# Performance work log

Measured on AMD Instinct MI355X. Metric: run time of the kernel, lower is better.

The kernel has to match this reference:

```python
import jax, jax.numpy as jnp
import numpy as np

D = 1024  # 2 * hidden_size

def setup_inputs() -> dict:
    key = jax.random.key(0)
    ks = jax.random.split(key, 7)
    s = 1.0 / np.sqrt(D)
    return {
        "lstm_output": jax.random.normal(ks[0], (8, 2048, D), dtype=jnp.float32),
        "Wq": jax.random.uniform(ks[1], (D, D), jnp.float32, -s, s),
        "bq": jax.random.uniform(ks[2], (D,), jnp.float32, -s, s),
        "Wk": jax.random.uniform(ks[3], (D, D), jnp.float32, -s, s),
        "bk": jax.random.uniform(ks[4], (D,), jnp.float32, -s, s),
        "Wv": jax.random.uniform(ks[5], (D, D), jnp.float32, -s, s),
        "bv": jax.random.uniform(ks[6], (D,), jnp.float32, -s, s),
    }

def reference(lstm_output, Wq, bq, Wk, bk, Wv, bv):
    # x: [B, S, D]
    Q = lstm_output @ Wq + bq
    K = lstm_output @ Wk + bk
    V = lstm_output @ Wv + bv
    # Unscaled attention scores: [B, S, S]
    scores = jnp.einsum("bqd,bkd->bqk", Q, K)
    weights = jax.nn.softmax(scores, axis=-1)
    context = jnp.einsum("bqk,bkd->bqd", weights, V)
    return context
```

## Files before the change

### kernel.cpp

```cpp
#include <hip/hip_runtime.h>

typedef _Float16 half8 __attribute__((ext_vector_type(8)));
typedef _Float16 half4 __attribute__((ext_vector_type(4)));
typedef short short8 __attribute__((ext_vector_type(8)));
typedef unsigned short ushort4v __attribute__((ext_vector_type(4)));
typedef float floatx4 __attribute__((ext_vector_type(4)));

#define ASYNC16(g, l) __builtin_amdgcn_global_load_lds( \
    (const __attribute__((address_space(1))) void*)(g),  \
    (__attribute__((address_space(3))) void*)(l), 16, 0, 0)

__device__ inline unsigned short f2bf(float f) {
    unsigned u = __builtin_bit_cast(unsigned, f);
    u += 0x7fff + ((u >> 16) & 1);
    return (unsigned short)(u >> 16);
}
__device__ inline float bf2f(unsigned short b) {
    unsigned u = (unsigned)b << 16;
    return __builtin_bit_cast(float, u);
}

__global__ void cvt_f2h(const float* __restrict__ in, _Float16* __restrict__ out, int n4)
{
    int i = blockIdx.x * blockDim.x + threadIdx.x;
    const int stride = gridDim.x * blockDim.x;
    for (; i < n4; i += stride) {
        float4 v = ((const float4*)in)[i];
        half4 h = { (_Float16)v.x, (_Float16)v.y, (_Float16)v.z, (_Float16)v.w };
        ((half4*)out)[i] = h;
    }
}

__global__ void transpose_w(const float* __restrict__ Wq, const float* __restrict__ Wk,
                            const float* __restrict__ Wv, _Float16* __restrict__ Wt)
{
    const float* W = (blockIdx.z == 0) ? Wq : (blockIdx.z == 1) ? Wk : Wv;
    _Float16* out = Wt + (size_t)blockIdx.z * 1024 * 1024;
    __shared__ float t[32][33];
    const int tx = threadIdx.x, ty = threadIdx.y;
    const int k0 = blockIdx.x * 32, n0 = blockIdx.y * 32;
#pragma unroll
    for (int i = 0; i < 32; i += 8)
        t[ty + i][tx] = W[(size_t)(k0 + ty + i) * 1024 + n0 + tx];
    __syncthreads();
#pragma unroll
    for (int i = 0; i < 32; i += 8)
        out[(size_t)(n0 + ty + i) * 1024 + k0 + tx] = (_Float16)t[tx][ty + i];
}

__global__ __launch_bounds__(256, 2)
void gemm_qkv(const _Float16* __restrict__ X, const _Float16* __restrict__ Wt,
              const float* __restrict__ bq, const float* __restrict__ bk,
              const float* __restrict__ bv,
              _Float16* __restrict__ Qh, _Float16* __restrict__ Kh,
              unsigned short* __restrict__ Vt)
{
    __shared__ __align__(16) _Float16 sA[128 * 64];
    __shared__ __align__(16) _Float16 sB[128 * 64];
    const int tid = threadIdx.x;
    const int lane = tid & 63, wave = tid >> 6;
    const int quad = lane >> 4, l15 = lane & 15;
    const int wm = (wave & 1) * 64, wn = (wave >> 1) * 64;
    const long m0 = (long)blockIdx.y * 128;
    const int  n0 = blockIdx.x * 128;

    const _Float16* Ab = X + m0 * 1024;
    const _Float16* Bb = Wt + (long)n0 * 1024;

    long offA[4];
    int ldsOff[4];
#pragma unroll
    for (int u = 0; u < 4; ++u) {
        const int c = tid + u * 256;
        const int row = c >> 3, g = (c & 7) ^ (row & 7);
        offA[u] = (long)row * 1024 + g * 8;
        ldsOff[u] = c * 16;
    }
    const int sw = l15 & 7;

    floatx4 acc[4][4] = {};

    for (int k0 = 0; k0 < 1024; k0 += 64) {
        __syncthreads();
#pragma unroll
        for (int u = 0; u < 4; ++u) {
            ASYNC16(Ab + offA[u] + k0, (char*)sA + ldsOff[u]);
            ASYNC16(Bb + offA[u] + k0, (char*)sB + ldsOff[u]);
        }
        __syncthreads();
#pragma unroll
        for (int s = 0; s < 2; ++s) {
            const int ck = ((s * 4 + quad) ^ sw) * 8;
            half8 af[4], bf[4];
#pragma unroll
            for (int i = 0; i < 4; ++i) {
                af[i] = *(const half8*)(sA + (wm + i * 16 + l15) * 64 + ck);
                bf[i] = *(const half8*)(sB + (wn + i * 16 + l15) * 64 + ck);
            }
#pragma unroll
            for (int i = 0; i < 4; ++i)
#pragma unroll
                for (int j = 0; j < 4; ++j)
                    acc[i][j] = __builtin_amdgcn_mfma_f32_16x16x32_f16(af[i], bf[j], acc[i][j], 0, 0, 0);
        }
    }

    const int which = n0 >> 10;
    const int ncol0 = n0 & 1023;
    const float* bias = (which == 0) ? bq : (which == 1) ? bk : bv;

    if (which < 2) {
        _Float16* O = which ? Kh : Qh;
#pragma unroll
        for (int i = 0; i < 4; ++i) {
            const long mb = m0 + wm + i * 16 + quad * 4;
#pragma unroll
            for (int j = 0; j < 4; ++j) {
                const int col = ncol0 + wn + j * 16 + l15;
                const float bb = bias[col];
                _Float16* op = O + mb * 1024 + col;
#pragma unroll
                for (int r = 0; r < 4; ++r)
                    op[(long)r * 1024] = (_Float16)(acc[i][j][r] + bb);
            }
        }
    } else {
#pragma unroll
        for (int i = 0; i < 4; ++i) {
            const long mb = m0 + wm + i * 16 + quad * 4;
            const int b = (int)(mb >> 11);
            const int s = (int)(mb & 2047);
#pragma unroll
            for (int j = 0; j < 4; ++j) {
                const int col = ncol0 + wn + j * 16 + l15;
                const float bb = bias[col];
                ushort4v h;
#pragma unroll
                for (int r = 0; r < 4; ++r) h[r] = f2bf(acc[i][j][r] + bb);
                *(ushort4v*)(Vt + (long)b * 2097152 + (long)col * 2048 + s) = h;
            }
        }
    }
}

__global__ __launch_bounds__(256, 2)
void gemm_sc(const _Float16* __restrict__ Q, const _Float16* __restrict__ K,
             unsigned short* __restrict__ E, float* __restrict__ rowsum)
{
    __shared__ __align__(16) _Float16 sA[128 * 64];
    __shared__ __align__(16) _Float16 sB[128 * 64];
    const int tid = threadIdx.x;
    const int lane = tid & 63, wave = tid >> 6;
    const int quad = lane >> 4, l15 = lane & 15;
    const int wm = (wave & 1) * 64, wn = (wave >> 1) * 64;
    const long m0 = (long)blockIdx.y * 128;
    const long n0 = (long)blockIdx.x * 128;

    const _Float16* Ab = Q + (long)blockIdx.z * 2097152 + m0 * 1024;
    const _Float16* Bb = K + (long)blockIdx.z * 2097152 + n0 * 1024;
    unsigned short* Eb = E + (long)blockIdx.z * 4194304;
    float* rs = rowsum + (long)blockIdx.z * 2048;

    long offA[4];
    int ldsOff[4];
#pragma unroll
    for (int u = 0; u < 4; ++u) {
        const int c = tid + u * 256;
        const int row = c >> 3, g = (c & 7) ^ (row & 7);
        offA[u] = (long)row * 1024 + g * 8;
        ldsOff[u] = c * 16;
    }
    const int sw = l15 & 7;

    floatx4 acc[4][4] = {};

    for (int k0 = 0; k0 < 1024; k0 += 64) {
        __syncthreads();
#pragma unroll
        for (int u = 0; u < 4; ++u) {
            ASYNC16(Ab + offA[u] + k0, (char*)sA + ldsOff[u]);
            ASYNC16(Bb + offA[u] + k0, (char*)sB + ldsOff[u]);
        }
        __syncthreads();
#pragma unroll
        for (int s = 0; s < 2; ++s) {
            const int ck = ((s * 4 + quad) ^ sw) * 8;
            half8 af[4], bf[4];
#pragma unroll
            for (int i = 0; i < 4; ++i) {
                af[i] = *(const half8*)(sA + (wm + i * 16 + l15) * 64 + ck);
                bf[i] = *(const half8*)(sB + (wn + i * 16 + l15) * 64 + ck);
            }
#pragma unroll
            for (int i = 0; i < 4; ++i)
#pragma unroll
                for (int j = 0; j < 4; ++j)
                    acc[i][j] = __builtin_amdgcn_mfma_f32_16x16x32_f16(af[i], bf[j], acc[i][j], 0, 0, 0);
        }
    }

#pragma unroll
    for (int i = 0; i < 4; ++i) {
        const int rowb = (int)(m0 + wm + i * 16 + quad * 4);
#pragma unroll
        for (int r = 0; r < 4; ++r) {
            float sl = 0.f;
#pragma unroll
            for (int j = 0; j < 4; ++j) {
                const long col = n0 + wn + j * 16 + l15;
                unsigned short b = f2bf(__expf(acc[i][j][r] - 40.0f));
                Eb[(long)(rowb + r) * 2048 + col] = b;
                sl += bf2f(b);
            }
            sl += __shfl_xor(sl, 1);
            sl += __shfl_xor(sl, 2);
            sl += __shfl_xor(sl, 4);
            sl += __shfl_xor(sl, 8);
            if (l15 == 0) atomicAdd(&rs[rowb + r], sl);
        }
    }
}

__global__ __launch_bounds__(256, 2)
void gemm_pv(const unsigned short* __restrict__ E, const unsigned short* __restrict__ Vt,
             const float* __restrict__ rowsum, float* __restrict__ C)
{
    __shared__ __align__(16) unsigned short sA[128 * 64];
    __shared__ __align__(16) unsigned short sB[128 * 64];
    const int tid = threadIdx.x;
    const int lane = tid & 63, wave = tid >> 6;
    const int quad = lane >> 4, l15 = lane & 15;
    const int wm = (wave & 1) * 64, wn = (wave >> 1) * 64;
    const long m0 = (long)blockIdx.y * 128;
    const long n0 = (long)blockIdx.x * 128;

    const unsigned short* Ab = E + (long)blockIdx.z * 4194304 + m0 * 2048;
    const unsigned short* Bb = Vt + (long)blockIdx.z * 2097152 + n0 * 2048;
    const float* rs = rowsum + (long)blockIdx.z * 2048;
    float* Cb = C + (long)blockIdx.z * 2097152;

    long offA[4];
    int ldsOff[4];
#pragma unroll
    for (int u = 0; u < 4; ++u) {
        const int c = tid + u * 256;
        const int row = c >> 3, g = (c & 7) ^ (row & 7);
        offA[u] = (long)row * 2048 + g * 8;
        ldsOff[u] = c * 16;
    }
    const int sw = l15 & 7;

    floatx4 acc[4][4] = {};

    for (int k0 = 0; k0 < 2048; k0 += 64) {
        __syncthreads();
#pragma unroll
        for (int u = 0; u < 4; ++u) {
            ASYNC16(Ab + offA[u] + k0, (char*)sA + ldsOff[u]);
            ASYNC16(Bb + offA[u] + k0, (char*)sB + ldsOff[u]);
        }
        __syncthreads();
#pragma unroll
        for (int s = 0; s < 2; ++s) {
            const int ck = ((s * 4 + quad) ^ sw) * 8;
            short8 af[4], bf[4];
#pragma unroll
            for (int i = 0; i < 4; ++i) {
                af[i] = *(const short8*)(sA + (wm + i * 16 + l15) * 64 + ck);
                bf[i] = *(const short8*)(sB + (wn + i * 16 + l15) * 64 + ck);
            }
#pragma unroll
            for (int i = 0; i < 4; ++i)
#pragma unroll
                for (int j = 0; j < 4; ++j)
                    acc[i][j] = __builtin_amdgcn_mfma_f32_16x16x32_bf16(af[i], bf[j], acc[i][j], 0, 0, 0);
        }
    }

#pragma unroll
    for (int i = 0; i < 4; ++i) {
        const int rowb = (int)(m0 + wm + i * 16 + quad * 4);
#pragma unroll
        for (int r = 0; r < 4; ++r) {
            const float inv = 1.0f / rs[rowb + r];
            float* cp = Cb + (long)(rowb + r) * 1024 + n0 + wn + l15;
#pragma unroll
            for (int j = 0; j < 4; ++j)
                cp[j * 16] = acc[i][j][r] * inv;
        }
    }
}

extern "C" void kernel_launch(void* const* d_in, const int* in_sizes, int n_in,
                              void* d_out, int out_size, void* d_ws, size_t ws_size,
                              hipStream_t stream)
{
    const float* x  = (const float*)d_in[0];
    const float* Wq = (const float*)d_in[1];
    const float* bq = (const float*)d_in[2];
    const float* Wk = (const float*)d_in[3];
    const float* bk = (const float*)d_in[4];
    const float* Wv = (const float*)d_in[5];
    const float* bv = (const float*)d_in[6];
    float* out = (float*)d_out;

    char* ws = (char*)d_ws;
    _Float16* Qh = (_Float16*)ws;
    _Float16* Kh = Qh + 16777216;
    unsigned short* Vt = (unsigned short*)(Kh + 16777216);
    char* region = ws + 100663296;
    _Float16* xh = (_Float16*)region;
    _Float16* Wt = xh + 16777216;
    unsigned short* E = (unsigned short*)region;

    int c = 8;
    size_t region_sz;
    for (;;) {
        region_sz = (size_t)c * 8388608ull;
        if (region_sz < 39845888ull) region_sz = 39845888ull;
        if (100663296ull + region_sz + 65536ull <= ws_size || c == 1) break;
        c >>= 1;
    }
    float* rowsum = (float*)(ws + 100663296 + region_sz);

    cvt_f2h<<<2048, 256, 0, stream>>>(x, xh, 16777216 / 4);
    transpose_w<<<dim3(32, 32, 3), dim3(32, 8, 1), 0, stream>>>(Wq, Wk, Wv, Wt);
    gemm_qkv<<<dim3(24, 128, 1), 256, 0, stream>>>(xh, Wt, bq, bk, bv, Qh, Kh, Vt);

    for (int b0 = 0; b0 < 8; b0 += c) {
        int cc = (8 - b0 < c) ? (8 - b0) : c;
        hipMemsetAsync(rowsum, 0, (size_t)cc * 2048 * 4, stream);
        gemm_sc<<<dim3(16, 16, cc), 256, 0, stream>>>(
            Qh + (long)b0 * 2097152, Kh + (long)b0 * 2097152, E, rowsum);
        gemm_pv<<<dim3(8, 16, cc), 256, 0, stream>>>(
            E, Vt + (long)b0 * 2097152, rowsum, out + (long)b0 * 2097152);
    }
}
```

Before: 412.2 us.

## Rewrite GEMMs as 256x256 eight-wave double-buffered pipelined kernels

All three GEMM kernels (QKV projection, scores, PV) now share one core: 256x256 output tiles, 512 threads (8 waves) and 128KB of dynamic LDS. Async global-to-LDS loads are double-buffered and interleaved with MFMA blocks using explicit waitcnt, barrier and setprio scheduling. A block-index remap spreads neighbouring tiles across XCDs for cache locality. The goals are more operand reuse per load and overlap of memory latency with matrix math. In exchange, occupancy drops to one workgroup per CU, register pressure rises, and the hand-written waitcnt counts must match the loads exactly.

```diff
diff --git a/kernel.cpp b/kernel.cpp
--- a/kernel.cpp
+++ b/kernel.cpp
@@ -48,62 +48,146 @@
         out[(size_t)(n0 + ty + i) * 1024 + k0 + tx] = (_Float16)t[tx][ty + i];
 }
 
-__global__ __launch_bounds__(256, 2)
-void gemm_qkv(const _Float16* __restrict__ X, const _Float16* __restrict__ Wt,
-              const float* __restrict__ bq, const float* __restrict__ bk,
-              const float* __restrict__ bv,
-              _Float16* __restrict__ Qh, _Float16* __restrict__ Kh,
-              unsigned short* __restrict__ Vt)
-{
-    __shared__ __align__(16) _Float16 sA[128 * 64];
-    __shared__ __align__(16) _Float16 sB[128 * 64];
+template<bool BF16>
+__device__ __forceinline__ floatx4 MF(short8 a, short8 b, floatx4 c) {
+    if constexpr (BF16)
+        return __builtin_amdgcn_mfma_f32_16x16x32_bf16(a, b, c, 0, 0, 0);
+    else
+        return __builtin_amdgcn_mfma_f32_16x16x32_f16(
+            __builtin_bit_cast(half8, a), __builtin_bit_cast(half8, b), c, 0, 0, 0);
+}
+
+template<int LDA, int LDB, int NT, bool BF16>
+__device__ __forceinline__ void gemm_core8(
+    const unsigned short* __restrict__ Ab, const unsigned short* __restrict__ Bb,
+    unsigned short* sA, unsigned short* sB, floatx4 (&acc)[8][4])
+{
     const int tid = threadIdx.x;
-    const int lane = tid & 63, wave = tid >> 6;
-    const int quad = lane >> 4, l15 = lane & 15;
-    const int wm = (wave & 1) * 64, wn = (wave >> 1) * 64;
-    const long m0 = (long)blockIdx.y * 128;
-    const int  n0 = blockIdx.x * 128;
-
-    const _Float16* Ab = X + m0 * 1024;
-    const _Float16* Bb = Wt + (long)n0 * 1024;
-
-    long offA[4];
-    int ldsOff[4];
-#pragma unroll
-    for (int u = 0; u < 4; ++u) {
-        const int c = tid + u * 256;
-        const int row = c >> 3, g = (c & 7) ^ (row & 7);
-        offA[u] = (long)row * 1024 + g * 8;
-        ldsOff[u] = c * 16;
-    }
+    const int lane = tid & 63, quad = lane >> 4, l15 = lane & 15;
+    const int wave = tid >> 6;
+    const int wm = wave >> 2, wn = wave & 3;
+    const int rowbase = wm * 128, colbase = wn * 64;
     const int sw = l15 & 7;
 
-    floatx4 acc[4][4] = {};
-
-    for (int k0 = 0; k0 < 1024; k0 += 64) {
-        __syncthreads();
-#pragma unroll
-        for (int u = 0; u < 4; ++u) {
-            ASYNC16(Ab + offA[u] + k0, (char*)sA + ldsOff[u]);
-            ASYNC16(Bb + offA[u] + k0, (char*)sB + ldsOff[u]);
-        }
-        __syncthreads();
-#pragma unroll
-        for (int s = 0; s < 2; ++s) {
-            const int ck = ((s * 4 + quad) ^ sw) * 8;
-            half8 af[4], bf[4];
-#pragma unroll
-            for (int i = 0; i < 4; ++i) {
-                af[i] = *(const half8*)(sA + (wm + i * 16 + l15) * 64 + ck);
-                bf[i] = *(const half8*)(sB + (wn + i * 16 + l15) * 64 + ck);
-            }
-#pragma unroll
-            for (int i = 0; i < 4; ++i)
-#pragma unroll
-                for (int j = 0; j < 4; ++j)
-                    acc[i][j] = __builtin_amdgcn_mfma_f32_16x16x32_f16(af[i], bf[j], acc[i][j], 0, 0, 0);
-        }
-    }
+    long srcA[2], srcB[2];
+    int dst[2];
+#pragma unroll
+    for (int u = 0; u < 2; ++u) {
+        const int c = tid + u * 512;
+        const int row = c >> 3;
+        const int g = (c & 7) ^ (row & 7);
+        srcA[u] = (long)row * LDA + g * 8;
+        srcB[u] = (long)row * LDB + g * 8;
+        dst[u] = c * 16;
+    }
+
+    short8 a[4][2], b[2][2][2];
+
+    auto stgA = [&](int p, int h, int kt) {
+#pragma unroll
+        for (int u = 0; u < 2; ++u)
+            ASYNC16(Ab + (long)kt * 64 + (long)h * (128 * LDA) + srcA[u],
+                    (char*)sA + p * 32768 + h * 16384 + dst[u]);
+    };
+    auto stgB = [&](int p, int h, int kt) {
+#pragma unroll
+        for (int u = 0; u < 2; ++u)
+            ASYNC16(Bb + (long)kt * 64 + (long)h * (128 * LDB) + srcB[u],
+                    (char*)sB + p * 32768 + h * 16384 + dst[u]);
+    };
+    auto rdA = [&](int mq, int p) {
+#pragma unroll
+        for (int ii = 0; ii < 4; ++ii) {
+            const int row = rowbase + (mq * 4 + ii) * 16 + l15;
+#pragma unroll
+            for (int kk = 0; kk < 2; ++kk)
+                a[ii][kk] = *(const short8*)(sA + p * 16384 + row * 64 +
+                                             (((kk * 4 + quad) ^ sw) * 8));
+        }
+    };
+    auto rdB = [&](int nq, int p) {
+#pragma unroll
+        for (int jj = 0; jj < 2; ++jj) {
+            const int row = colbase + (nq * 2 + jj) * 16 + l15;
+#pragma unroll
+            for (int kk = 0; kk < 2; ++kk)
+                b[nq][jj][kk] = *(const short8*)(sB + p * 16384 + row * 64 +
+                                                 (((kk * 4 + quad) ^ sw) * 8));
+        }
+    };
+    auto mm = [&](int mq, int nq) {
+        __builtin_amdgcn_s_setprio(1);
+#pragma unroll
+        for (int ii = 0; ii < 4; ++ii)
+#pragma unroll
+            for (int jj = 0; jj < 2; ++jj)
+#pragma unroll
+                for (int kk = 0; kk < 2; ++kk)
+                    acc[mq * 4 + ii][nq * 2 + jj] =
+                        MF<BF16>(a[ii][kk], b[nq][jj][kk], acc[mq * 4 + ii][nq * 2 + jj]);
+        __builtin_amdgcn_s_setprio(0);
+    };
+    auto bar   = [] { __builtin_amdgcn_s_barrier(); };
+    auto lgkm0 = [] { asm volatile("s_waitcnt lgkmcnt(0)" ::: "memory");
+                      __builtin_amdgcn_sched_barrier(0); };
+    auto vm4   = [] { asm volatile("s_waitcnt vmcnt(4)" ::: "memory"); };
+    auto vm8   = [] { asm volatile("s_waitcnt vmcnt(8)" ::: "memory"); };
+
+    stgA(0, 0, 0); stgA(0, 1, 0); stgB(0, 0, 0); stgB(0, 1, 0);
+    stgA(1, 0, 1); stgA(1, 1, 1); stgB(1, 0, 1); stgB(1, 1, 1);
+    vm8();
+    bar();
+
+#pragma unroll 1
+    for (int i = 0; i < NT / 2; ++i) {
+        const int t2 = (2 * i + 2) & (NT - 1);
+        const int t3 = (2 * i + 3) & (NT - 1);
+        rdA(0, 0); rdB(0, 0);
+        bar(); lgkm0(); mm(0, 0); bar();
+        rdB(1, 0);
+        bar(); lgkm0(); mm(0, 1); bar();
+        rdA(1, 0); stgB(0, 0, t2);
+        bar(); lgkm0(); mm(1, 1); bar();
+        stgB(0, 1, t2); vm4();
+        bar(); mm(1, 0); bar();
+        rdA(0, 1); rdB(0, 1); stgA(0, 0, t2);
+        bar(); lgkm0(); mm(0, 0); bar();
+        rdB(1, 1); stgA(0, 1, t2);
+        bar(); lgkm0(); mm(0, 1); bar();
+        rdA(1, 1); stgB(1, 0, t3);
+        bar(); lgkm0(); mm(1, 1); bar();
+        stgB(1, 1, t3); stgA(1, 0, t3); stgA(1, 1, t3);
+        vm8();
+        bar(); mm(1, 0); bar();
+    }
+    asm volatile("s_waitcnt vmcnt(0)" ::: "memory");
+}
+
+__global__ __launch_bounds__(512, 2)
+void gemm_qkv8(const unsigned short* __restrict__ X, const unsigned short* __restrict__ Wt,
+               const float* __restrict__ bq, const float* __restrict__ bk,
+               const float* __restrict__ bv,
+               _Float16* __restrict__ Qh, _Float16* __restrict__ Kh,
+               unsigned short* __restrict__ Vt)
+{
+    extern __shared__ unsigned short smem[];
+    unsigned short* sA = smem;
+    unsigned short* sB = smem + 32768;
+
+    constexpr int GX = 12, GY = 64, NWG = GX * GY;
+    const int d = blockIdx.y * GX + blockIdx.x;
+    const int wf = (d & 7) * (NWG >> 3) + (d >> 3);
+    const int bx = wf % GX, by = wf / GX;
+
+    const long m0 = (long)by * 256;
+    const int n0 = bx * 256;
+
+    floatx4 acc[8][4] = {};
+    gemm_core8<1024, 1024, 16, false>(X + m0 * 1024, Wt + (long)n0 * 1024, sA, sB, acc);
+
+    const int tid = threadIdx.x;
+    const int lane = tid & 63, quad = lane >> 4, l15 = lane & 15;
+    const int wave = tid >> 6, wm = wave >> 2, wn = wave & 3;
 
     const int which = n0 >> 10;
     const int ncol0 = n0 & 1023;
@@ -112,11 +196,11 @@
     if (which < 2) {
         _Float16* O = which ? Kh : Qh;
 #pragma unroll
-        for (int i = 0; i < 4; ++i) {
-            const long mb = m0 + wm + i * 16 + quad * 4;
+        for (int i = 0; i < 8; ++i) {
+            const long mb = m0 + wm * 128 + i * 16 + quad * 4;
 #pragma unroll
             for (int j = 0; j < 4; ++j) {
-                const int col = ncol0 + wn + j * 16 + l15;
+                const int col = ncol0 + wn * 64 + j * 16 + l15;
                 const float bb = bias[col];
                 _Float16* op = O + mb * 1024 + col;
 #pragma unroll
@@ -126,91 +210,61 @@
         }
     } else {
 #pragma unroll
-        for (int i = 0; i < 4; ++i) {
-            const long mb = m0 + wm + i * 16 + quad * 4;
-            const int b = (int)(mb >> 11);
+        for (int i = 0; i < 8; ++i) {
+            const long mb = m0 + wm * 128 + i * 16 + quad * 4;
+            const int bz = (int)(mb >> 11);
             const int s = (int)(mb & 2047);
 #pragma unroll
             for (int j = 0; j < 4; ++j) {
-                const int col = ncol0 + wn + j * 16 + l15;
+                const int col = ncol0 + wn * 64 + j * 16 + l15;
                 const float bb = bias[col];
                 ushort4v h;
 #pragma unroll
                 for (int r = 0; r < 4; ++r) h[r] = f2bf(acc[i][j][r] + bb);
-                *(ushort4v*)(Vt + (long)b * 2097152 + (long)col * 2048 + s) = h;
+                *(ushort4v*)(Vt + (long)bz * 2097152 + (long)col * 2048 + s) = h;
             }
         }
     }
 }
 
-__global__ __launch_bounds__(256, 2)
-void gemm_sc(const _Float16* __restrict__ Q, const _Float16* __restrict__ K,
-             unsigned short* __restrict__ E, float* __restrict__ rowsum)
-{
-    __shared__ __align__(16) _Float16 sA[128 * 64];
-    __shared__ __align__(16) _Float16 sB[128 * 64];
-    const int tid = threadIdx.x;
-    const int lane = tid & 63, wave = tid >> 6;
-    const int quad = lane >> 4, l15 = lane & 15;
-    const int wm = (wave & 1) * 64, wn = (wave >> 1) * 64;
-    const long m0 = (long)blockIdx.y * 128;
-    const long n0 = (long)blockIdx.x * 128;
-
-    const _Float16* Ab = Q + (long)blockIdx.z * 2097152 + m0 * 1024;
-    const _Float16* Bb = K + (long)blockIdx.z * 2097152 + n0 * 1024;
+__global__ __launch_bounds__(512, 2)
+void gemm_sc8(const unsigned short* __restrict__ Q, const unsigned short* __restrict__ K,
+              unsigned short* __restrict__ E, float* __restrict__ rowsum)
+{
+    extern __shared__ unsigned short smem[];
+    unsigned short* sA = smem;
+    unsigned short* sB = smem + 32768;
+
+    constexpr int GX = 8, GY = 8, NWG = GX * GY;
+    const int d = blockIdx.y * GX + blockIdx.x;
+    const int wf = (d & 7) * (NWG >> 3) + (d >> 3);
+    const int bx = wf % GX, by = wf / GX;
+
+    const long m0 = (long)by * 256;
+    const long n0 = (long)bx * 256;
+    const long zo = (long)blockIdx.z * 2097152;
     unsigned short* Eb = E + (long)blockIdx.z * 4194304;
     float* rs = rowsum + (long)blockIdx.z * 2048;
 
-    long offA[4];
-    int ldsOff[4];
-#pragma unroll
-    for (int u = 0; u < 4; ++u) {
-        const int c = tid + u * 256;
-        const int row = c >> 3, g = (c & 7) ^ (row & 7);
-        offA[u] = (long)row * 1024 + g * 8;
-        ldsOff[u] = c * 16;
-    }
-    const int sw = l15 & 7;
-
-    floatx4 acc[4][4] = {};
-
-    for (int k0 = 0; k0 < 1024; k0 += 64) {
-        __syncthreads();
-#pragma unroll
-        for (int u = 0; u < 4; ++u) {
-            ASYNC16(Ab + offA[u] + k0, (char*)sA + ldsOff[u]);
-            ASYNC16(Bb + offA[u] + k0, (char*)sB + ldsOff[u]);
-        }
-        __syncthreads();
-#pragma unroll
-        for (int s = 0; s < 2; ++s) {
-            const int ck = ((s * 4 + quad) ^ sw) * 8;
-            half8 af[4], bf[4];
-#pragma unroll
-            for (int i = 0; i < 4; ++i) {
-                af[i] = *(const half8*)(sA + (wm + i * 16 + l15) * 64 + ck);
-                bf[i] = *(const half8*)(sB + (wn + i * 16 + l15) * 64 + ck);
-            }
-#pragma unroll
-            for (int i = 0; i < 4; ++i)
-#pragma unroll
-                for (int j = 0; j < 4; ++j)
-                    acc[i][j] = __builtin_amdgcn_mfma_f32_16x16x32_f16(af[i], bf[j], acc[i][j], 0, 0, 0);
-        }
-    }
-
-#pragma unroll
-    for (int i = 0; i < 4; ++i) {
-        const int rowb = (int)(m0 + wm + i * 16 + quad * 4);
+    floatx4 acc[8][4] = {};
+    gemm_core8<1024, 1024, 16, false>(Q + zo + m0 * 1024, K + zo + n0 * 1024, sA, sB, acc);
+
+    const int tid = threadIdx.x;
+    const int lane = tid & 63, quad = lane >> 4, l15 = lane & 15;
+    const int wave = tid >> 6, wm = wave >> 2, wn = wave & 3;
+
+#pragma unroll
+    for (int i = 0; i < 8; ++i) {
+        const int rowb = (int)m0 + wm * 128 + i * 16 + quad * 4;
 #pragma unroll
         for (int r = 0; r < 4; ++r) {
             float sl = 0.f;
 #pragma unroll
             for (int j = 0; j < 4; ++j) {
-                const long col = n0 + wn + j * 16 + l15;
-                unsigned short b = f2bf(__expf(acc[i][j][r] - 40.0f));
-                Eb[(long)(rowb + r) * 2048 + col] = b;
-                sl += bf2f(b);
+                const long col = n0 + wn * 64 + j * 16 + l15;
+                const unsigned short bb = f2bf(__expf(acc[i][j][r] - 40.0f));
+                Eb[(long)(rowb + r) * 2048 + col] = bb;
+                sl += bf2f(bb);
             }
             sl += __shfl_xor(sl, 1);
             sl += __shfl_xor(sl, 2);
@@ -221,69 +275,41 @@
     }
 }
 
-__global__ __launch_bounds__(256, 2)
-void gemm_pv(const unsigned short* __restrict__ E, const unsigned short* __restrict__ Vt,
-             const float* __restrict__ rowsum, float* __restrict__ C)
-{
-    __shared__ __align__(16) unsigned short sA[128 * 64];
-    __shared__ __align__(16) unsigned short sB[128 * 64];
-    const int tid = threadIdx.x;
-    const int lane = tid & 63, wave = tid >> 6;
-    const int quad = lane >> 4, l15 = lane & 15;
-    const int wm = (wave & 1) * 64, wn = (wave >> 1) * 64;
-    const long m0 = (long)blockIdx.y * 128;
-    const long n0 = (long)blockIdx.x * 128;
+__global__ __launch_bounds__(512, 2)
+void gemm_pv8(const unsigned short* __restrict__ E, const unsigned short* __restrict__ Vt,
+              const float* __restrict__ rowsum, float* __restrict__ C)
+{
+    extern __shared__ unsigned short smem[];
+    unsigned short* sA = smem;
+    unsigned short* sB = smem + 32768;
+
+    constexpr int GX = 4, GY = 8, NWG = GX * GY;
+    const int d = blockIdx.y * GX + blockIdx.x;
+    const int wf = (d & 7) * (NWG >> 3) + (d >> 3);
+    const int bx = wf % GX, by = wf / GX;
+
+    const long m0 = (long)by * 256;
+    const long n0 = (long)bx * 256;
 
     const unsigned short* Ab = E + (long)blockIdx.z * 4194304 + m0 * 2048;
     const unsigned short* Bb = Vt + (long)blockIdx.z * 2097152 + n0 * 2048;
     const float* rs = rowsum + (long)blockIdx.z * 2048;
     float* Cb = C + (long)blockIdx.z * 2097152;
 
-    long offA[4];
-    int ldsOff[4];
-#pragma unroll
-    for (int u = 0; u < 4; ++u) {
-        const int c = tid + u * 256;
-        const int row = c >> 3, g = (c & 7) ^ (row & 7);
-        offA[u] = (long)row * 2048 + g * 8;
-        ldsOff[u] = c * 16;
-    }
-    const int sw = l15 & 7;
-
-    floatx4 acc[4][4] = {};
-
-    for (int k0 = 0; k0 < 2048; k0 += 64) {
-        __syncthreads();
-#pragma unroll
-        for (int u = 0; u < 4; ++u) {
-            ASYNC16(Ab + offA[u] + k0, (char*)sA + ldsOff[u]);
-            ASYNC16(Bb + offA[u] + k0, (char*)sB + ldsOff[u]);
-        }
-        __syncthreads();
-#pragma unroll
-        for (int s = 0; s < 2; ++s) {
-            const int ck = ((s * 4 + quad) ^ sw) * 8;
-            short8 af[4], bf[4];
-#pragma unroll
-            for (int i = 0; i < 4; ++i) {
-                af[i] = *(const short8*)(sA + (wm + i * 16 + l15) * 64 + ck);
-                bf[i] = *(const short8*)(sB + (wn + i * 16 + l15) * 64 + ck);
-            }
-#pragma unroll
-            for (int i = 0; i < 4; ++i)
-#pragma unroll
-                for (int j = 0; j < 4; ++j)
-                    acc[i][j] = __builtin_amdgcn_mfma_f32_16x16x32_bf16(af[i], bf[j], acc[i][j], 0, 0, 0);
-        }
-    }
-
-#pragma unroll
-    for (int i = 0; i < 4; ++i) {
-        const int rowb = (int)(m0 + wm + i * 16 + quad * 4);
+    floatx4 acc[8][4] = {};
+    gemm_core8<2048, 2048, 32, true>(Ab, Bb, sA, sB, acc);
+
+    const int tid = threadIdx.x;
+    const int lane = tid & 63, quad = lane >> 4, l15 = lane & 15;
+    const int wave = tid >> 6, wm = wave >> 2, wn = wave & 3;
+
+#pragma unroll
+    for (int i = 0; i < 8; ++i) {
+        const int rowb = (int)m0 + wm * 128 + i * 16 + quad * 4;
 #pragma unroll
         for (int r = 0; r < 4; ++r) {
             const float inv = 1.0f / rs[rowb + r];
-            float* cp = Cb + (long)(rowb + r) * 1024 + n0 + wn + l15;
+            float* cp = Cb + (long)(rowb + r) * 1024 + n0 + wn * 64 + l15;
 #pragma unroll
             for (int j = 0; j < 4; ++j)
                 cp[j * 16] = acc[i][j][r] * inv;
@@ -323,16 +349,29 @@
     }
     float* rowsum = (float*)(ws + 100663296 + region_sz);
 
+    static bool attr_done = false;
+    if (!attr_done) {
+        hipFuncSetAttribute((const void*)gemm_qkv8,
+                            hipFuncAttributeMaxDynamicSharedMemorySize, 131072);
+        hipFuncSetAttribute((const void*)gemm_sc8,
+                            hipFuncAttributeMaxDynamicSharedMemorySize, 131072);
+        hipFuncSetAttribute((const void*)gemm_pv8,
+                            hipFuncAttributeMaxDynamicSharedMemorySize, 131072);
+        attr_done = true;
+    }
+
     cvt_f2h<<<2048, 256, 0, stream>>>(x, xh, 16777216 / 4);
     transpose_w<<<dim3(32, 32, 3), dim3(32, 8, 1), 0, stream>>>(Wq, Wk, Wv, Wt);
-    gemm_qkv<<<dim3(24, 128, 1), 256, 0, stream>>>(xh, Wt, bq, bk, bv, Qh, Kh, Vt);
+    gemm_qkv8<<<dim3(12, 64, 1), 512, 131072, stream>>>(
+        (const unsigned short*)xh, (const unsigned short*)Wt, bq, bk, bv, Qh, Kh, Vt);
 
     for (int b0 = 0; b0 < 8; b0 += c) {
         int cc = (8 - b0 < c) ? (8 - b0) : c;
         hipMemsetAsync(rowsum, 0, (size_t)cc * 2048 * 4, stream);
-        gemm_sc<<<dim3(16, 16, cc), 256, 0, stream>>>(
-            Qh + (long)b0 * 2097152, Kh + (long)b0 * 2097152, E, rowsum);
-        gemm_pv<<<dim3(8, 16, cc), 256, 0, stream>>>(
+        gemm_sc8<<<dim3(8, 8, cc), 512, 131072, stream>>>(
+            (const unsigned short*)(Qh + (long)b0 * 2097152),
+            (const unsigned short*)(Kh + (long)b0 * 2097152), E, rowsum);
+        gemm_pv8<<<dim3(4, 8, cc), 512, 131072, stream>>>(
             E, Vt + (long)b0 * 2097152, rowsum, out + (long)b0 * 2097152);
     }
 }
```

Result: faster. 390.1 us (-5.4%).
